# Performance work log

Measured on AMD Instinct MI355X. Metric: run time of the kernel, lower is better.

## Reference

```python
import jax, jax.numpy as jnp
import numpy as np

THETA = 10000.0

def _rope(x, pos):
    # x: [b, h, s, hd]; pos: [s]
    hd = x.shape[-1]
    inv_freq = 1.0 / (THETA ** (jnp.arange(0, hd, 2, dtype=jnp.float32) / hd))  # [hd/2]
    ang = pos.astype(jnp.float32)[:, None] * inv_freq[None, :]                   # [s, hd/2]
    cos, sin = jnp.cos(ang), jnp.sin(ang)
    x1, x2 = x[..., 0::2], x[..., 1::2]
    r1 = x1 * cos - x2 * sin
    r2 = x1 * sin + x2 * cos
    return jnp.stack([r1, r2], axis=-1).reshape(x.shape)

def setup_inputs() -> dict:
    key = jax.random.key(0)
    ks = jax.random.split(key, 5)
    b, s, d = 2, 2048, 1024
    scale = 0.02
    return {
        "x": jax.random.normal(ks[0], (b, s, d), dtype=jnp.float32),
        "Wq": jax.random.normal(ks[1], (d, d), dtype=jnp.float32) * scale,
        "Wk": jax.random.normal(ks[2], (d, d), dtype=jnp.float32) * scale,
        "Wv": jax.random.normal(ks[3], (d, d), dtype=jnp.float32) * scale,
        "Wo": jax.random.normal(ks[4], (d, d), dtype=jnp.float32) * scale,
    }

def reference(x, Wq, Wk, Wv, Wo):
    b, s, d = x.shape
    n_heads = 16
    hd = d // n_heads

    def split_heads(t):  # [b,s,d] -> [b,h,s,hd]
        return t.reshape(b, s, n_heads, hd).transpose(0, 2, 1, 3)

    q = split_heads(x @ Wq.T)
    k = split_heads(x @ Wk.T)
    v = split_heads(x @ Wv.T)

    pos = jnp.arange(s)
    q = _rope(q, pos)
    k = _rope(k, pos)

    scores = jnp.einsum("bhqd,bhkd->bhqk", q, k) / jnp.sqrt(jnp.float32(hd))
    causal = jnp.tril(jnp.ones((s, s), dtype=bool))
    scores = jnp.where(causal, scores, -jnp.inf)
    attn = jax.nn.softmax(scores, axis=-1)
    ctx = jnp.einsum("bhqk,bhkd->bhqd", attn, v)
    ctx = ctx.transpose(0, 2, 1, 3).reshape(b, s, d)
    return ctx @ Wo.T
```

## Files before the change

kernel.cpp:

```cpp
#include <hip/hip_runtime.h>
#include <math.h>

#define B  2
#define S  2048
#define D  1024
#define NH 16
#define HD 64
#define NROWS (B * S)

#define AS1 __attribute__((address_space(1)))
#define AS3 __attribute__((address_space(3)))
#define GLD16(g, l) __builtin_amdgcn_global_load_lds((const AS1 void*)(g), (AS3 void*)(l), 16, 0, 0)

typedef __attribute__((ext_vector_type(8))) short short8;
typedef __attribute__((ext_vector_type(4))) float floatx4;

#define MFMA16(a, b, c) __builtin_amdgcn_mfma_f32_16x16x32_bf16((a), (b), (c), 0, 0, 0)

__device__ inline unsigned short f2bf(float f) {
    union { float f; unsigned int u; } v; v.f = f;
    unsigned int u = v.u;
    u += 0x7fffu + ((u >> 16) & 1);
    return (unsigned short)(u >> 16);
}

__global__ __launch_bounds__(256) void cvt_kernel(
    const float* __restrict__ x,  const float* __restrict__ Wq,
    const float* __restrict__ Wk, const float* __restrict__ Wv,
    const float* __restrict__ Wo,
    unsigned short* __restrict__ xb,  unsigned short* __restrict__ wqb,
    unsigned short* __restrict__ wkb, unsigned short* __restrict__ wvb,
    unsigned short* __restrict__ wob)
{
    size_t idx = (size_t)blockIdx.x * 256 + threadIdx.x;
    const float* src; unsigned short* dst; size_t off;
    if (idx < (1u << 20)) { src = x; dst = xb; off = idx << 2; }
    else {
        size_t r = idx - (1u << 20);
        int w = (int)(r >> 18);
        off = (r & ((1u << 18) - 1)) << 2;
        src = (w == 0) ? Wq : (w == 1) ? Wk : (w == 2) ? Wv : Wo;
        dst = (w == 0) ? wqb : (w == 1) ? wkb : (w == 2) ? wvb : wob;
    }
    float4 f = *(const float4*)(src + off);
    ushort4 o;
    o.x = f2bf(f.x); o.y = f2bf(f.y); o.z = f2bf(f.z); o.w = f2bf(f.w);
    *(ushort4*)(dst + off) = o;
}

#define GEMM_STAGE(Abase, Bbase, kk, AD, BD)                                   \
{                                                                              \
    GLD16(Abase + (size_t)row0 * D + (kk) + ko0, AD + seg0 * 512);             \
    GLD16(Abase + (size_t)row1 * D + (kk) + ko1, AD + (seg0 + 1) * 512);       \
    GLD16(Bbase + (size_t)row0 * D + (kk) + ko0, BD + seg0 * 512);             \
    GLD16(Bbase + (size_t)row1 * D + (kk) + ko1, BD + (seg0 + 1) * 512);       \
}

#define GEMM_COMPUTE(AC, BC)                                                   \
{                                                                              \
    short8 a[4], b[4];                                                         \
    _Pragma("unroll")                                                          \
    for (int mi = 0; mi < 4; ++mi)                                             \
        a[mi] = *(const short8*)&AC[(wm + mi * 16 + lm) * 32 + quad * 8];      \
    _Pragma("unroll")                                                          \
    for (int ni = 0; ni < 4; ++ni)                                             \
        b[ni] = *(const short8*)&BC[(wn + ni * 16 + lm) * 32 + quad * 8];      \
    _Pragma("unroll")                                                          \
    for (int mi = 0; mi < 4; ++mi)                                             \
        _Pragma("unroll")                                                      \
        for (int ni = 0; ni < 4; ++ni)                                         \
            acc[mi][ni] = MFMA16(b[ni], a[mi], acc[mi][ni]);      \
}

__global__ __launch_bounds__(256) void gemm_qkv_mfma(
    const unsigned short* __restrict__ xb,
    const unsigned short* __restrict__ wqb,
    const unsigned short* __restrict__ wkb,
    const unsigned short* __restrict__ wvb,
    unsigned short* __restrict__ Qo, unsigned short* __restrict__ Ko,
    unsigned short* __restrict__ Vo)
{
    __shared__ short As0[128 * 32];
    __shared__ short As1[128 * 32];
    __shared__ short Bs0[128 * 32];
    __shared__ short Bs1[128 * 32];

    const int t    = threadIdx.x;
    const int wave = t >> 6, lane = t & 63;
    const int i0   = blockIdx.x * 128;
    const int by   = blockIdx.y;
    const int mat  = by >> 3;
    const int j0   = (by & 7) * 128;
    const unsigned short* __restrict__ W = (mat == 0) ? wqb : (mat == 1) ? wkb : wvb;
    unsigned short* __restrict__ out = (mat == 0) ? Qo : (mat == 1) ? Ko : Vo;

    const int wm = (wave & 1) * 64, wn = (wave >> 1) * 64;
    const int lm = lane & 15, quad = lane >> 4;

    const int seg0 = wave * 2;
    const int c0   = seg0 * 64 + lane;
    const int row0 = c0 >> 2, ko0 = (c0 & 3) << 3;
    const int c1   = c0 + 64;
    const int row1 = c1 >> 2, ko1 = (c1 & 3) << 3;

    const unsigned short* Abase = xb + (size_t)i0 * D;
    const unsigned short* Bbase = W  + (size_t)j0 * D;

    floatx4 acc[4][4] = {};

    GEMM_STAGE(Abase, Bbase, 0, As0, Bs0);
    __syncthreads();
    for (int k0 = 0; k0 < D; k0 += 64) {
        GEMM_STAGE(Abase, Bbase, k0 + 32, As1, Bs1);
        GEMM_COMPUTE(As0, Bs0);
        __syncthreads();
        if (k0 + 64 < D) GEMM_STAGE(Abase, Bbase, k0 + 64, As0, Bs0);
        GEMM_COMPUTE(As1, Bs1);
        __syncthreads();
    }

    const int h = (j0 + wn) >> 6;
    #pragma unroll
    for (int mi = 0; mi < 4; ++mi) {
        const int mg = i0 + wm + mi * 16 + lm;
        const int si = mg & (S - 1), bb = mg >> 11;
        unsigned short* orow = out + ((size_t)(bb * NH + h) * S + si) * HD;
        #pragma unroll
        for (int ni = 0; ni < 4; ++ni) {
            const int dim0 = ni * 16 + quad * 4;
            floatx4 v = acc[mi][ni];
            ushort4 pk;
            if (mat < 2) {
                float rv[4];
                #pragma unroll
                for (int p = 0; p < 2; ++p) {
                    float invf = exp2f(-(float)(dim0 + 2 * p) *
                                       (13.287712379549449f / 64.0f));
                    float sn, cs;
                    __sincosf((float)si * invf, &sn, &cs);
                    float x1 = v[2 * p], x2 = v[2 * p + 1];
                    float r1 = x1 * cs - x2 * sn;
                    float r2 = x1 * sn + x2 * cs;
                    if (mat == 0) {
                        r1 *= 0.1803368801111204f;
                        r2 *= 0.1803368801111204f;
                    }
                    rv[2 * p] = r1; rv[2 * p + 1] = r2;
                }
                pk.x = f2bf(rv[0]); pk.y = f2bf(rv[1]);
                pk.z = f2bf(rv[2]); pk.w = f2bf(rv[3]);
            } else {
                pk.x = f2bf(v[0]); pk.y = f2bf(v[1]);
                pk.z = f2bf(v[2]); pk.w = f2bf(v[3]);
            }
            *(ushort4*)(orow + dim0) = pk;
        }
    }
}

__global__ __launch_bounds__(256) void gemm_out_mfma(
    const unsigned short* __restrict__ Cb,
    const unsigned short* __restrict__ wob,
    float* __restrict__ out)
{
    __shared__ short As0[128 * 32];
    __shared__ short As1[128 * 32];
    __shared__ short Bs0[128 * 32];
    __shared__ short Bs1[128 * 32];

    const int t    = threadIdx.x;
    const int wave = t >> 6, lane = t & 63;
    const int i0   = blockIdx.x * 128;
    const int j0   = blockIdx.y * 128;

    const int wm = (wave & 1) * 64, wn = (wave >> 1) * 64;
    const int lm = lane & 15, quad = lane >> 4;

    const int seg0 = wave * 2;
    const int c0   = seg0 * 64 + lane;
    const int row0 = c0 >> 2, ko0 = (c0 & 3) << 3;
    const int c1   = c0 + 64;
    const int row1 = c1 >> 2, ko1 = (c1 & 3) << 3;

    const unsigned short* Abase = Cb  + (size_t)i0 * D;
    const unsigned short* Bbase = wob + (size_t)j0 * D;

    floatx4 acc[4][4] = {};

    GEMM_STAGE(Abase, Bbase, 0, As0, Bs0);
    __syncthreads();
    for (int k0 = 0; k0 < D; k0 += 64) {
        GEMM_STAGE(Abase, Bbase, k0 + 32, As1, Bs1);
        GEMM_COMPUTE(As0, Bs0);
        __syncthreads();
        if (k0 + 64 < D) GEMM_STAGE(Abase, Bbase, k0 + 64, As0, Bs0);
        GEMM_COMPUTE(As1, Bs1);
        __syncthreads();
    }

    #pragma unroll
    for (int mi = 0; mi < 4; ++mi) {
        const int mg = i0 + wm + mi * 16 + lm;
        float* orow = out + (size_t)mg * D;
        #pragma unroll
        for (int ni = 0; ni < 4; ++ni) {
            const int ng = j0 + wn + ni * 16 + quad * 4;
            *(floatx4*)(orow + ng) = acc[mi][ni];
        }
    }
}

__global__ __launch_bounds__(256) void vtrans_kernel(
    const unsigned short* __restrict__ Vb, unsigned short* __restrict__ Vt)
{
    __shared__ unsigned short T[64][72];
    const int t  = threadIdx.x;
    const int st = blockIdx.x, bh = blockIdx.y;
    const unsigned short* src = Vb + ((size_t)bh * S + st * 64) * HD;

    #pragma unroll
    for (int i = 0; i < 2; ++i) {
        int c = t + i * 256;
        int s = c & 63, dp = c >> 6;
        short8 v = *(const short8*)(src + (size_t)s * HD + dp * 8);
        #pragma unroll
        for (int j = 0; j < 8; ++j)
            T[dp * 8 + j][s] = (unsigned short)v[j];
    }
    __syncthreads();
    unsigned short* dst = Vt + (size_t)bh * HD * S + (size_t)st * 64;
    #pragma unroll
    for (int i = 0; i < 2; ++i) {
        int c = t + i * 256;
        int d = c >> 3, sp = (c & 7) * 8;
        short8 v = *(const short8*)&T[d][sp];
        *(short8*)(dst + (size_t)d * S + sp) = v;
    }
}

#define ATTN_STEP(KC, VC, KN, VN)                                              \
{                                                                              \
    _Pragma("unroll")                                                          \
    for (int i = 0; i < 2; ++i) {                                              \
        int c = t + i * 256;                                                   \
        int row = c >> 3;                                                      \
        int dkc = (c & 7) ^ (row & 7);                                         \
        GLD16(Kg + (size_t)(k0n + row) * HD + dkc * 8, &KN[0][0] + c * 8);     \
        GLD16(Vg + (size_t)row * S + k0n + dkc * 8,    &VN[0][0] + c * 8);     \
    }                                                                          \
    short8 kb0[4], kb1[4];                                                     \
    _Pragma("unroll")                                                          \
    for (int nt = 0; nt < 4; ++nt) {                                           \
        kb0[nt] = *(const short8*)&KC[nt * 16 + lm][(quad ^ sw) * 8];          \
        kb1[nt] = *(const short8*)&KC[nt * 16 + lm][((4 + quad) ^ sw) * 8];    \
    }                                                                          \
    floatx4 sc[4];                                                             \
    _Pragma("unroll")                                                          \
    for (int nt = 0; nt < 4; ++nt) {                                           \
        floatx4 s = {0.f, 0.f, 0.f, 0.f};                                      \
        s = MFMA16(qa0, kb0[nt], s);                                           \
        s = MFMA16(qa1, kb1[nt], s);                                           \
        sc[nt] = s;                                                            \
    }                                                                          \
    if (diag) {                                                                \
        _Pragma("unroll")                                                      \
        for (int r = 0; r < 4; ++r)                                            \
            _Pragma("unroll")                                                  \
            for (int nt = 0; nt < 4; ++nt) {                                   \
                float pe = exp2f(sc[nt][r]);                                   \
                if (nt * 16 + lm > 16 * wave + quad * 4 + r) pe = 0.0f;        \
                sc[nt][r] = pe;                                                \
                lsum[r] += pe;                                                 \
            }                                                                  \
    } else {                                                                   \
        _Pragma("unroll")                                                      \
        for (int r = 0; r < 4; ++r)                                            \
            _Pragma("unroll")                                                  \
            for (int nt = 0; nt < 4; ++nt) {                                   \
                float pe = exp2f(sc[nt][r]);                                   \
                sc[nt][r] = pe;                                                \
                lsum[r] += pe;                                                 \
            }                                                                  \
    }                                                                          \
    _Pragma("unroll")                                                          \
    for (int nt = 0; nt < 4; ++nt)                                             \
        _Pragma("unroll")                                                      \
        for (int r = 0; r < 4; ++r) {                                          \
            int q = 16 * wave + quad * 4 + r;                                  \
            Ps[q][(((nt * 2 + (lm >> 3)) ^ (q & 7)) * 8) + (lm & 7)] =         \
                f2bf(sc[nt][r]);                                               \
        }                                                                      \
    short8 pa0 = *(const short8*)&Ps[16 * wave + lm][(quad ^ sw) * 8];         \
    short8 pa1 = *(const short8*)&Ps[16 * wave + lm][((4 + quad) ^ sw) * 8];   \
    _Pragma("unroll")                                                          \
    for (int nt = 0; nt < 4; ++nt) {                                           \
        short8 vb0 = *(const short8*)&VC[nt * 16 + lm][(quad ^ sw) * 8];       \
        short8 vb1 = *(const short8*)&VC[nt * 16 + lm][((4 + quad) ^ sw) * 8]; \
        o[nt] = MFMA16(pa0, vb0, o[nt]);                                       \
        o[nt] = MFMA16(pa1, vb1, o[nt]);                                       \
    }                                                                          \
    __syncthreads();                                                           \
}

__global__ __launch_bounds__(256, 4) void attn_mfma(
    const unsigned short* __restrict__ Qb,
    const unsigned short* __restrict__ Kb,
    const unsigned short* __restrict__ Vt,
    unsigned short* __restrict__ Cb)
{
    __shared__ unsigned short Ks0[64][64];
    __shared__ unsigned short Ks1[64][64];
    __shared__ unsigned short Vs0[64][64];
    __shared__ unsigned short Vs1[64][64];
    __shared__ unsigned short Ps[64][64];

    const int t    = threadIdx.x;
    const int lane = t & 63, wave = t >> 6;
    const int lm   = lane & 15, quad = lane >> 4;
    const int sw   = lm & 7;

    const int b     = blockIdx.x;
    const int bh    = b & 31;
    const int f     = (b >> 5) & 7;
    const int round = b >> 8;
    int qt;
    if      (round == 0) qt = f;
    else if (round == 1) qt = 15 - f;
    else if (round == 2) qt = 16 + f;
    else                 qt = 31 - f;
    const int q0 = qt * 64;

    const unsigned short* Qg = Qb + (size_t)bh * S * HD;
    const unsigned short* Kg = Kb + (size_t)bh * S * HD;
    const unsigned short* Vg = Vt + (size_t)bh * HD * S;

    short8 qa0 = *(const short8*)(Qg + (size_t)(q0 + 16 * wave + lm) * HD + quad * 8);
    short8 qa1 = *(const short8*)(Qg + (size_t)(q0 + 16 * wave + lm) * HD + 32 + quad * 8);

    #pragma unroll
    for (int i = 0; i < 2; ++i) {
        int c = t + i * 256;
        int row = c >> 3;
        int dkc = (c & 7) ^ (row & 7);
        GLD16(Kg + (size_t)row * HD + dkc * 8, &Ks0[0][0] + c * 8);
        GLD16(Vg + (size_t)row * S + dkc * 8,  &Vs0[0][0] + c * 8);
    }

    float lsum[4] = {0.f, 0.f, 0.f, 0.f};
    floatx4 o[4] = {};

    __syncthreads();

    for (int kt = 0; kt <= qt; ++kt) {
        const int k0n = (kt + 1) * 64;
        const bool diag = (kt == qt);
        if ((kt & 1) == 0) ATTN_STEP(Ks0, Vs0, Ks1, Vs1)
        else               ATTN_STEP(Ks1, Vs1, Ks0, Vs0)
    }

    #pragma unroll
    for (int r = 0; r < 4; ++r) {
        #pragma unroll
        for (int off = 1; off < 16; off <<= 1)
            lsum[r] += __shfl_xor(lsum[r], off);
    }
    const int h = bh & (NH - 1), bb = bh >> 4;
    #pragma unroll
    for (int r = 0; r < 4; ++r) {
        float inv = 1.0f / lsum[r];
        size_t row = (size_t)bb * S + q0 + 16 * wave + quad * 4 + r;
        #pragma unroll
        for (int nt = 0; nt < 4; ++nt)
            Cb[row * D + h * HD + nt * 16 + lm] = f2bf(o[nt][r] * inv);
    }
}

extern "C" void kernel_launch(void* const* d_in, const int* in_sizes, int n_in,
                              void* d_out, int out_size, void* d_ws, size_t ws_size,
                              hipStream_t stream) {
    (void)in_sizes; (void)n_in; (void)out_size; (void)ws_size;
    const float* x  = (const float*)d_in[0];
    const float* Wq = (const float*)d_in[1];
    const float* Wk = (const float*)d_in[2];
    const float* Wv = (const float*)d_in[3];
    const float* Wo = (const float*)d_in[4];
    float* out = (float*)d_out;

    char* w = (char*)d_ws;
    unsigned short* Qb  = (unsigned short*)(w);
    unsigned short* Kb  = (unsigned short*)(w + (((size_t)8)  << 20));
    unsigned short* Vb  = (unsigned short*)(w + (((size_t)16) << 20));
    unsigned short* Vtb = (unsigned short*)(w + (((size_t)24) << 20));
    unsigned short* Cb  = (unsigned short*)(w + (((size_t)32) << 20));
    unsigned short* xb  = (unsigned short*)(w + (((size_t)40) << 20));
    unsigned short* wqb = (unsigned short*)(w + (((size_t)48) << 20));
    unsigned short* wkb = (unsigned short*)(w + (((size_t)50) << 20));
    unsigned short* wvb = (unsigned short*)(w + (((size_t)52) << 20));
    unsigned short* wob = (unsigned short*)(w + (((size_t)54) << 20));

    cvt_kernel<<<8192, 256, 0, stream>>>(x, Wq, Wk, Wv, Wo,
                                         xb, wqb, wkb, wvb, wob);

    dim3 g1(NROWS / 128, 24);
    gemm_qkv_mfma<<<g1, 256, 0, stream>>>(xb, wqb, wkb, wvb, Qb, Kb, Vb);

    dim3 gt(S / 64, B * NH);
    vtrans_kernel<<<gt, 256, 0, stream>>>(Vb, Vtb);

    attn_mfma<<<1024, 256, 0, stream>>>(Qb, Kb, Vtb, Cb);

    dim3 g3(NROWS / 128, D / 128);
    gemm_out_mfma<<<g3, 256, 0, stream>>>(Cb, wob, out);
}
```

Measured before the change: 192.8 us.

## Fuse V transpose into QKV GEMM epilogue and transpose score MFMA layout

The QKV GEMM now writes V directly in transposed [bh, hd, s] layout, which removes the separate vtrans kernel launch and its extra read and write of V. The attention kernel swaps the MFMA operand order so each lane holds scores for one query row. That lets the P tile be written to LDS as packed ushort4 with a new swizzle, and the row sum becomes a single per-lane scalar reduced with two shuffles. The risk is that the transposed V store is scattered 2-byte writes with stride S, which may coalesce poorly.

```diff
diff --git a/kernel.cpp b/kernel.cpp
--- a/kernel.cpp
+++ b/kernel.cpp
@@ -120,17 +120,16 @@
     }
 
     const int h = (j0 + wn) >> 6;
-    #pragma unroll
-    for (int mi = 0; mi < 4; ++mi) {
-        const int mg = i0 + wm + mi * 16 + lm;
-        const int si = mg & (S - 1), bb = mg >> 11;
-        unsigned short* orow = out + ((size_t)(bb * NH + h) * S + si) * HD;
+    if (mat < 2) {
         #pragma unroll
-        for (int ni = 0; ni < 4; ++ni) {
-            const int dim0 = ni * 16 + quad * 4;
-            floatx4 v = acc[mi][ni];
-            ushort4 pk;
-            if (mat < 2) {
+        for (int mi = 0; mi < 4; ++mi) {
+            const int mg = i0 + wm + mi * 16 + lm;
+            const int si = mg & (S - 1), bb = mg >> 11;
+            unsigned short* orow = out + ((size_t)(bb * NH + h) * S + si) * HD;
+            #pragma unroll
+            for (int ni = 0; ni < 4; ++ni) {
+                const int dim0 = ni * 16 + quad * 4;
+                floatx4 v = acc[mi][ni];
                 float rv[4];
                 #pragma unroll
                 for (int p = 0; p < 2; ++p) {
@@ -147,13 +146,26 @@
                     }
                     rv[2 * p] = r1; rv[2 * p + 1] = r2;
                 }
+                ushort4 pk;
                 pk.x = f2bf(rv[0]); pk.y = f2bf(rv[1]);
                 pk.z = f2bf(rv[2]); pk.w = f2bf(rv[3]);
-            } else {
-                pk.x = f2bf(v[0]); pk.y = f2bf(v[1]);
-                pk.z = f2bf(v[2]); pk.w = f2bf(v[3]);
+                *(ushort4*)(orow + dim0) = pk;
             }
-            *(ushort4*)(orow + dim0) = pk;
+        }
+    } else {
+        #pragma unroll
+        for (int mi = 0; mi < 4; ++mi) {
+            const int mg = i0 + wm + mi * 16 + lm;
+            const int si = mg & (S - 1), bb = mg >> 11;
+            unsigned short* vb = out + (size_t)(bb * NH + h) * HD * S + si;
+            #pragma unroll
+            for (int ni = 0; ni < 4; ++ni) {
+                #pragma unroll
+                for (int p = 0; p < 4; ++p) {
+                    const int d = ni * 16 + quad * 4 + p;
+                    vb[(size_t)d * S] = f2bf(acc[mi][ni][p]);
+                }
+            }
         }
     }
 }
@@ -210,34 +222,6 @@
     }
 }
 
-__global__ __launch_bounds__(256) void vtrans_kernel(
-    const unsigned short* __restrict__ Vb, unsigned short* __restrict__ Vt)
-{
-    __shared__ unsigned short T[64][72];
-    const int t  = threadIdx.x;
-    const int st = blockIdx.x, bh = blockIdx.y;
-    const unsigned short* src = Vb + ((size_t)bh * S + st * 64) * HD;
-
-    #pragma unroll
-    for (int i = 0; i < 2; ++i) {
-        int c = t + i * 256;
-        int s = c & 63, dp = c >> 6;
-        short8 v = *(const short8*)(src + (size_t)s * HD + dp * 8);
-        #pragma unroll
-        for (int j = 0; j < 8; ++j)
-            T[dp * 8 + j][s] = (unsigned short)v[j];
-    }
-    __syncthreads();
-    unsigned short* dst = Vt + (size_t)bh * HD * S + (size_t)st * 64;
-    #pragma unroll
-    for (int i = 0; i < 2; ++i) {
-        int c = t + i * 256;
-        int d = c >> 3, sp = (c & 7) * 8;
-        short8 v = *(const short8*)&T[d][sp];
-        *(short8*)(dst + (size_t)d * S + sp) = v;
-    }
-}
-
 #define ATTN_STEP(KC, VC, KN, VN)                                              \
 {                                                                              \
     _Pragma("unroll")                                                          \
@@ -258,40 +242,40 @@
     _Pragma("unroll")                                                          \
     for (int nt = 0; nt < 4; ++nt) {                                           \
         floatx4 s = {0.f, 0.f, 0.f, 0.f};                                      \
-        s = MFMA16(qa0, kb0[nt], s);                                           \
-        s = MFMA16(qa1, kb1[nt], s);                                           \
+        s = MFMA16(kb0[nt], qa0, s);                \
+        s = MFMA16(kb1[nt], qa1, s);                                           \
         sc[nt] = s;                                                            \
     }                                                                          \
     if (diag) {                                                                \
         _Pragma("unroll")                                                      \
-        for (int r = 0; r < 4; ++r)                                            \
+        for (int nt = 0; nt < 4; ++nt)                                         \
             _Pragma("unroll")                                                  \
-            for (int nt = 0; nt < 4; ++nt) {                                   \
+            for (int r = 0; r < 4; ++r) {                                      \
                 float pe = exp2f(sc[nt][r]);                                   \
-                if (nt * 16 + lm > 16 * wave + quad * 4 + r) pe = 0.0f;        \
+                if (nt * 16 + quad * 4 + r > 16 * wave + lm) pe = 0.0f;        \
                 sc[nt][r] = pe;                                                \
-                lsum[r] += pe;                                                 \
+                lsum += pe;                                                    \
             }                                                                  \
     } else {                                                                   \
         _Pragma("unroll")                                                      \
-        for (int r = 0; r < 4; ++r)                                            \
+        for (int nt = 0; nt < 4; ++nt)                                         \
             _Pragma("unroll")                                                  \
-            for (int nt = 0; nt < 4; ++nt) {                                   \
+            for (int r = 0; r < 4; ++r) {                                      \
                 float pe = exp2f(sc[nt][r]);                                   \
                 sc[nt][r] = pe;                                                \
-                lsum[r] += pe;                                                 \
+                lsum += pe;                                                    \
             }                                                                  \
     }                                                                          \
     _Pragma("unroll")                                                          \
-    for (int nt = 0; nt < 4; ++nt)                                             \
-        _Pragma("unroll")                                                      \
-        for (int r = 0; r < 4; ++r) {                                          \
-            int q = 16 * wave + quad * 4 + r;                                  \
-            Ps[q][(((nt * 2 + (lm >> 3)) ^ (q & 7)) * 8) + (lm & 7)] =         \
-                f2bf(sc[nt][r]);                                               \
-        }                                                                      \
-    short8 pa0 = *(const short8*)&Ps[16 * wave + lm][(quad ^ sw) * 8];         \
-    short8 pa1 = *(const short8*)&Ps[16 * wave + lm][((4 + quad) ^ sw) * 8];   \
+    for (int nt = 0; nt < 4; ++nt) {                                           \
+        ushort4 pk;                                                            \
+        pk.x = f2bf(sc[nt][0]); pk.y = f2bf(sc[nt][1]);                        \
+        pk.z = f2bf(sc[nt][2]); pk.w = f2bf(sc[nt][3]);                        \
+        int cp = (nt * 4 + quad) ^ psw;                                        \
+        *(ushort4*)&Ps[16 * wave + lm][cp * 4] = pk;                           \
+    }                                                                          \
+    short8 pa0 = *(const short8*)&Ps[16 * wave + lm][((quad * 2) ^ psw) * 4];  \
+    short8 pa1 = *(const short8*)&Ps[16 * wave + lm][((8 + quad * 2) ^ psw) * 4]; \
     _Pragma("unroll")                                                          \
     for (int nt = 0; nt < 4; ++nt) {                                           \
         short8 vb0 = *(const short8*)&VC[nt * 16 + lm][(quad ^ sw) * 8];       \
@@ -318,6 +302,7 @@
     const int lane = t & 63, wave = t >> 6;
     const int lm   = lane & 15, quad = lane >> 4;
     const int sw   = lm & 7;
+    const int psw  = (lm & 7) << 1;
 
     const int b     = blockIdx.x;
     const int bh    = b & 31;
@@ -346,7 +331,7 @@
         GLD16(Vg + (size_t)row * S + dkc * 8,  &Vs0[0][0] + c * 8);
     }
 
-    float lsum[4] = {0.f, 0.f, 0.f, 0.f};
+    float lsum = 0.0f;
     floatx4 o[4] = {};
 
     __syncthreads();
@@ -358,16 +343,13 @@
         else               ATTN_STEP(Ks1, Vs1, Ks0, Vs0)
     }
 
-    #pragma unroll
-    for (int r = 0; r < 4; ++r) {
-        #pragma unroll
-        for (int off = 1; off < 16; off <<= 1)
-            lsum[r] += __shfl_xor(lsum[r], off);
-    }
+    lsum += __shfl_xor(lsum, 16);
+    lsum += __shfl_xor(lsum, 32);
     const int h = bh & (NH - 1), bb = bh >> 4;
     #pragma unroll
     for (int r = 0; r < 4; ++r) {
-        float inv = 1.0f / lsum[r];
+        float lr  = __shfl(lsum, (wave << 6 | (quad * 4 + r)) & 63);
+        float inv = 1.0f / lr;
         size_t row = (size_t)bb * S + q0 + 16 * wave + quad * 4 + r;
         #pragma unroll
         for (int nt = 0; nt < 4; ++nt)
@@ -389,23 +371,19 @@
     char* w = (char*)d_ws;
     unsigned short* Qb  = (unsigned short*)(w);
     unsigned short* Kb  = (unsigned short*)(w + (((size_t)8)  << 20));
-    unsigned short* Vb  = (unsigned short*)(w + (((size_t)16) << 20));
-    unsigned short* Vtb = (unsigned short*)(w + (((size_t)24) << 20));
-    unsigned short* Cb  = (unsigned short*)(w + (((size_t)32) << 20));
-    unsigned short* xb  = (unsigned short*)(w + (((size_t)40) << 20));
-    unsigned short* wqb = (unsigned short*)(w + (((size_t)48) << 20));
-    unsigned short* wkb = (unsigned short*)(w + (((size_t)50) << 20));
-    unsigned short* wvb = (unsigned short*)(w + (((size_t)52) << 20));
-    unsigned short* wob = (unsigned short*)(w + (((size_t)54) << 20));
+    unsigned short* Vtb = (unsigned short*)(w + (((size_t)16) << 20));
+    unsigned short* Cb  = (unsigned short*)(w + (((size_t)24) << 20));
+    unsigned short* xb  = (unsigned short*)(w + (((size_t)32) << 20));
+    unsigned short* wqb = (unsigned short*)(w + (((size_t)40) << 20));
+    unsigned short* wkb = (unsigned short*)(w + (((size_t)42) << 20));
+    unsigned short* wvb = (unsigned short*)(w + (((size_t)44) << 20));
+    unsigned short* wob = (unsigned short*)(w + (((size_t)46) << 20));
 
     cvt_kernel<<<8192, 256, 0, stream>>>(x, Wq, Wk, Wv, Wo,
                                          xb, wqb, wkb, wvb, wob);
 
     dim3 g1(NROWS / 128, 24);
-    gemm_qkv_mfma<<<g1, 256, 0, stream>>>(xb, wqb, wkb, wvb, Qb, Kb, Vb);
-
-    dim3 gt(S / 64, B * NH);
-    vtrans_kernel<<<gt, 256, 0, stream>>>(Vb, Vtb);
+    gemm_qkv_mfma<<<g1, 256, 0, stream>>>(xb, wqb, wkb, wvb, Qb, Kb, Vtb);
 
     attn_mfma<<<1024, 256, 0, stream>>>(Qb, Kb, Vtb, Cb);
 
```

After: 185.6 us. -3.7%, faster.
